# Kernel optimization log

Measured on AMD Instinct MI355X. Metric: run time of the kernel, lower is better.

The kernel has to match this reference:

```python
import jax, jax.numpy as jnp
import numpy as np

N, D, N_CLASSES = 8192, 512, 128
POS_MARGIN = 1.0  # default path: sample_method=None, Dynamic_margin=None


def setup_inputs() -> dict:
    key = jax.random.key(0)
    k1, k2 = jax.random.split(key)
    x = jax.random.normal(k1, (N, D), dtype=jnp.float32)
    # metric-learning embeddings are L2-normalized so sim in [-1, 1]
    x = x / jnp.linalg.norm(x, axis=1, keepdims=True)
    targets = jax.random.randint(k2, (N,), 0, N_CLASSES, dtype=jnp.int64)
    return {"inputs": x, "targets": targets, "nonorm": 0}


def reference(inputs, targets, nonorm):
    n = inputs.shape[0]
    sim = jnp.matmul(inputs, inputs.T)                      # [n, n]
    same = targets[:, None] == targets[None, :]             # [n, n]
    pos_mask = same & (sim < POS_MARGIN)                    # drops self-sim == 1
    neg_mask = ~same

    # per-row masked log-sum-exp (sort in original is irrelevant to the sums)
    pos_sum = jnp.sum(jnp.where(pos_mask, jnp.exp(1.0 - sim), 0.0), axis=1)
    neg_sum = jnp.sum(jnp.where(neg_mask, jnp.exp(sim), 0.0), axis=1)
    pos_loss = jnp.log(pos_sum)
    neg_loss = jnp.log(neg_sum)

    has_neg = jnp.any(neg_mask, axis=1)                     # rows w/o negs are skipped
    loss = jnp.sum(jnp.where(has_neg, pos_loss + neg_loss, 0.0)) / n
    prec = jnp.mean(1.0 - has_neg.astype(jnp.float32))      # fraction of skipped rows

    # torch code reports means of the LAST row's pos/neg pairs
    last_pos = pos_mask[-1]
    last_neg = neg_mask[-1]
    mean_pos_sim = jnp.sum(jnp.where(last_pos, sim[-1], 0.0)) / jnp.sum(last_pos)
    mean_neg_sim = jnp.sum(jnp.where(last_neg, sim[-1], 0.0)) / jnp.sum(last_neg)
    return loss, prec, mean_pos_sim, mean_neg_sim
```

## Files before the change

kernel.cpp:

```cpp
#include <hip/hip_runtime.h>
#include <math.h>

#define N_ 8192
#define D_ 512
#define NC_ 128
#define T_ 64
#define BK_ 32
#define KSTEPS 16

typedef __attribute__((ext_vector_type(8))) short bf16x8;
typedef __attribute__((ext_vector_type(4))) float f32x4;
typedef __attribute__((ext_vector_type(4))) unsigned short us4;

static __device__ __forceinline__ unsigned short f2bf(float f) {
    union { float f; unsigned u; } c; c.f = f;
    unsigned u = c.u;
    u += 0x7fffu + ((u >> 16) & 1u);
    return (unsigned short)(u >> 16);
}

__global__ __launch_bounds__(256) void k_pre(const float* __restrict__ x,
                                             unsigned short* __restrict__ xb,
                                             const int* __restrict__ tg,
                                             double* __restrict__ sim_last,
                                             int* __restrict__ hist32) {
    const int bid = blockIdx.x;
    const int tid = threadIdx.x;
    if (bid < 4096) {
        int i = bid * 256 + tid;
        float4 v = reinterpret_cast<const float4*>(x)[i];
        us4 o = { f2bf(v.x), f2bf(v.y), f2bf(v.z), f2bf(v.w) };
        reinterpret_cast<us4*>(xb)[i] = o;
    } else if (bid < 6144) {
        int j    = (bid - 4096) * 4 + (tid >> 6);
        int lane = tid & 63;
        const float* xl = x + (size_t)(N_ - 1) * D_;
        const float* xj = x + (size_t)j * D_;
        double acc = 0.0;
#pragma unroll
        for (int it = 0; it < 8; ++it) {
            int k = it * 64 + lane;
            acc += (double)xl[k] * (double)xj[k];
        }
#pragma unroll
        for (int m = 32; m >= 1; m >>= 1) acc += __shfl_xor(acc, m, 64);
        if (lane == 0) sim_last[j] = acc;
    } else {
        __shared__ int lh[NC_];
        int b = bid - 6144;
        if (tid < NC_) lh[tid] = 0;
        __syncthreads();
        atomicAdd(&lh[tg[b * 256 + tid]], 1);
        __syncthreads();
        if (tid < NC_) hist32[b * NC_ + tid] = lh[tid];
    }
}

__global__ __launch_bounds__(256, 4) void k_main(const unsigned short* __restrict__ xb,
                                                 const int* __restrict__ tg,
                                                 float* __restrict__ bufP,
                                                 float* __restrict__ bufN) {
    __shared__ alignas(16) unsigned short As[2][128 * BK_];
    __shared__ alignas(16) unsigned short Bs[2][128 * BK_];
    __shared__ int rowT[128];

    const int tid  = threadIdx.x;
    const int w    = tid >> 6;
    const int lane = tid & 63;
    const int q    = lane >> 4;
    const int l15  = lane & 15;
    const int wrow = w >> 1;
    const int wcol = w & 1;

    const int bswz = (blockIdx.x & 7) * 260 + (blockIdx.x >> 3);

    int rem = bswz;
    int it = 0;
    while (rem >= (T_ - it)) { rem -= (T_ - it); it++; }
    const int jt = it + rem;
    const int row0 = it * 128;
    const int col0 = jt * 128;

    auto STAGE = [&](int buf, int ks) {
        const int k0 = ks * BK_;
        unsigned short* Ad = As[buf];
        unsigned short* Bd = Bs[buf];
#pragma unroll
        for (int itr = 0; itr < 2; ++itr) {
            int slot = itr * 4 + w;
            int gs = slot * 64 + lane;
            int r  = gs >> 2;
            int sl = gs & 3;
            int g  = sl ^ ((r >> 1) & 3);
            const unsigned short* ga = xb + (size_t)(row0 + r) * D_ + k0 + g * 8;
            const unsigned short* gb = xb + (size_t)(col0 + r) * D_ + k0 + g * 8;
            __builtin_amdgcn_global_load_lds(
                (const __attribute__((address_space(1))) void*)ga,
                (__attribute__((address_space(3))) void*)(Ad + slot * 512),
                16, 0, 0);
            __builtin_amdgcn_global_load_lds(
                (const __attribute__((address_space(1))) void*)gb,
                (__attribute__((address_space(3))) void*)(Bd + slot * 512),
                16, 0, 0);
        }
    };

    if (tid < 128) rowT[tid] = tg[row0 + tid];
    STAGE(0, 0);
    __syncthreads();

    int tR[4][4];
#pragma unroll
    for (int mi = 0; mi < 4; ++mi)
#pragma unroll
        for (int r = 0; r < 4; ++r)
            tR[mi][r] = rowT[wrow * 64 + mi * 16 + q * 4 + r];

    int tC[4];
#pragma unroll
    for (int ni = 0; ni < 4; ++ni)
        tC[ni] = tg[col0 + wcol * 64 + ni * 16 + l15];

    f32x4 acc[4][4];
#pragma unroll
    for (int mi = 0; mi < 4; ++mi)
#pragma unroll
        for (int ni = 0; ni < 4; ++ni)
            acc[mi][ni] = (f32x4){0.f, 0.f, 0.f, 0.f};

    auto COMPUTE = [&](int buf) {
        const unsigned short* A = As[buf];
        const unsigned short* B = Bs[buf];
        bf16x8 aF[4], bF[4];
#pragma unroll
        for (int mi = 0; mi < 4; ++mi) {
            int rA = wrow * 64 + mi * 16 + l15;
            int sl = q ^ ((rA >> 1) & 3);
            aF[mi] = *reinterpret_cast<const bf16x8*>(A + rA * BK_ + sl * 8);
        }
#pragma unroll
        for (int ni = 0; ni < 4; ++ni) {
            int rB = wcol * 64 + ni * 16 + l15;
            int sl = q ^ ((rB >> 1) & 3);
            bF[ni] = *reinterpret_cast<const bf16x8*>(B + rB * BK_ + sl * 8);
        }
#pragma unroll
        for (int mi = 0; mi < 4; ++mi)
#pragma unroll
            for (int ni = 0; ni < 4; ++ni)
                acc[mi][ni] = __builtin_amdgcn_mfma_f32_16x16x32_bf16(
                    aF[mi], bF[ni], acc[mi][ni], 0, 0, 0);
    };

    int cur = 0;
#pragma unroll 1
    for (int ks = 0; ks < KSTEPS - 1; ++ks) {
        STAGE(cur ^ 1, ks + 1);
        COMPUTE(cur);
        __syncthreads();
        cur ^= 1;
    }
    COMPUTE(cur);

    float ps[4][4], ns[4][4];
    float cps[4], cns[4];
#pragma unroll
    for (int mi = 0; mi < 4; ++mi)
#pragma unroll
        for (int r = 0; r < 4; ++r) { ps[mi][r] = 0.f; ns[mi][r] = 0.f; }
#pragma unroll
    for (int ni = 0; ni < 4; ++ni) { cps[ni] = 0.f; cns[ni] = 0.f; }

#pragma unroll
    for (int mi = 0; mi < 4; ++mi)
#pragma unroll
        for (int ni = 0; ni < 4; ++ni)
#pragma unroll
            for (int r = 0; r < 4; ++r) {
                float s = acc[mi][ni][r];
                bool same = (tR[mi][r] == tC[ni]);
                float e = __expf(same ? 1.0f - s : s);
                float pe = (same && (s < 1.0f)) ? e : 0.0f;
                float ne = same ? 0.0f : e;
                ps[mi][r] += pe; ns[mi][r] += ne;
                cps[ni]   += pe; cns[ni]   += ne;
            }

    __syncthreads();
    float* scr = (float*)As;

#pragma unroll
    for (int mi = 0; mi < 4; ++mi)
#pragma unroll
        for (int r = 0; r < 4; ++r) {
            float p = ps[mi][r];
            float n = ns[mi][r];
#pragma unroll
            for (int m = 1; m < 16; m <<= 1) {
                p += __shfl_xor(p, m, 64);
                n += __shfl_xor(n, m, 64);
            }
            if (l15 == 0) {
                int rloc = wrow * 64 + mi * 16 + q * 4 + r;
                scr[wcol * 128 + rloc]       = p;
                scr[256 + wcol * 128 + rloc] = n;
            }
        }

#pragma unroll
    for (int ni = 0; ni < 4; ++ni) {
        float p = cps[ni];
        float n = cns[ni];
        p += __shfl_xor(p, 16, 64); p += __shfl_xor(p, 32, 64);
        n += __shfl_xor(n, 16, 64); n += __shfl_xor(n, 32, 64);
        if (q == 0) {
            int cloc = wcol * 64 + ni * 16 + l15;
            scr[512 + wrow * 128 + cloc] = p;
            scr[768 + wrow * 128 + cloc] = n;
        }
    }
    __syncthreads();

    if (tid < 128) {
        int r = tid;
        size_t off = ((size_t)it * T_ + jt) * 128 + r;
        bufP[off] = scr[r]       + scr[128 + r];
        bufN[off] = scr[256 + r] + scr[384 + r];
    } else if (jt != it) {
        int c = tid - 128;
        size_t off = ((size_t)jt * T_ + it) * 128 + c;
        bufP[off] = scr[512 + c] + scr[640 + c];
        bufN[off] = scr[768 + c] + scr[896 + c];
    }
}

__global__ __launch_bounds__(256) void k_reduce(const float* __restrict__ bufP,
                                                const float* __restrict__ bufN,
                                                const int* __restrict__ tg,
                                                const int* __restrict__ hist32,
                                                double* __restrict__ partd,
                                                int* __restrict__ skipc) {
    __shared__ float sv[256];
    __shared__ int lh[NC_];
    __shared__ double rd[128];
    __shared__ int ri[128];
    const int t   = blockIdx.x;
    const int tid = threadIdx.x;
    const int half = tid >> 7;
    const int r    = tid & 127;
    const float* buf = half ? bufN : bufP;
    const float* base = buf + (size_t)t * T_ * 128 + r;
    float s = 0.f;
#pragma unroll
    for (int o = 0; o < T_; ++o) s += base[o * 128];
    sv[tid] = s;
    if (tid < NC_) {
        int a = 0;
#pragma unroll
        for (int b = 0; b < 32; ++b) a += hist32[b * NC_ + tid];
        lh[tid] = a;
    }
    __syncthreads();
    if (tid < 128) {
        int row = t * 128 + tid;
        bool ok = lh[tg[row]] < N_;
        rd[tid] = ok ? (double)(logf(sv[tid]) + logf(sv[128 + tid])) : 0.0;
        ri[tid] = ok ? 0 : 1;
    }
    __syncthreads();
    for (int st = 64; st >= 1; st >>= 1) {
        if (tid < st) { rd[tid] += rd[tid + st]; ri[tid] += ri[tid + st]; }
        __syncthreads();
    }
    if (tid == 0) { partd[t] = rd[0]; skipc[t] = ri[0]; }
}

__global__ __launch_bounds__(1024) void k_final(const double* __restrict__ partd,
                                                const int* __restrict__ skipc,
                                                const int* __restrict__ tg,
                                                const double* __restrict__ sim_last,
                                                float* __restrict__ out) {
    __shared__ double sl[1024], sp[1024], sn[1024];
    __shared__ int    sk[1024], cp[1024], cn[1024];
    int tid = threadIdx.x;

    double part = (tid < 64) ? partd[tid] : 0.0;
    int    skip = (tid < 64) ? skipc[tid] : 0;

    double pd = 0.0, nd = 0.0;
    int pc = 0, nc = 0;
    int tlast = tg[N_ - 1];
    for (int j = tid; j < N_; j += 1024) {
        double s = sim_last[j];
        if (tg[j] == tlast) {
            if (s < 1.0) { pd += s; pc++; }
        } else {
            nd += s; nc++;
        }
    }

    sl[tid] = part; sk[tid] = skip;
    sp[tid] = pd;   cp[tid] = pc;
    sn[tid] = nd;   cn[tid] = nc;
    __syncthreads();
    for (int s = 512; s >= 1; s >>= 1) {
        if (tid < s) {
            sl[tid] += sl[tid + s]; sk[tid] += sk[tid + s];
            sp[tid] += sp[tid + s]; cp[tid] += cp[tid + s];
            sn[tid] += sn[tid + s]; cn[tid] += cn[tid + s];
        }
        __syncthreads();
    }
    if (tid == 0) {
        out[0] = (float)(sl[0] / (double)N_);
        out[1] = (float)sk[0] / (float)N_;
        out[2] = (float)(sp[0] / (double)cp[0]);
        out[3] = (float)(sn[0] / (double)cn[0]);
    }
}

extern "C" void kernel_launch(void* const* d_in, const int* in_sizes, int n_in,
                              void* d_out, int out_size, void* d_ws, size_t ws_size,
                              hipStream_t stream) {
    const float* x  = (const float*)d_in[0];
    const int*   tg = (const int*)d_in[1];
    char* ws = (char*)d_ws;

    unsigned short* xb = (unsigned short*)ws;
    const size_t XB = (size_t)N_ * D_ * 2;
    double* partd    = (double*)(ws + XB);
    int*    skipc    = (int*)(ws + XB + 512);
    int*    hist32   = (int*)(ws + XB + 1024);
    double* sim_last = (double*)(ws + XB + 65536);
    float*  bufP     = (float*)(ws + XB + 131072);
    float*  bufN     = (float*)(ws + XB + 131072 + 2097152);

    const int nblk_tri = T_ * (T_ + 1) / 2;

    hipLaunchKernelGGL(k_pre, dim3(4096 + 2048 + 32), dim3(256), 0, stream,
                       x, xb, tg, sim_last, hist32);
    hipLaunchKernelGGL(k_main, dim3(nblk_tri), dim3(256), 0, stream, xb, tg, bufP, bufN);
    hipLaunchKernelGGL(k_reduce, dim3(T_), dim3(256), 0, stream,
                       bufP, bufN, tg, hist32, partd, skipc);
    hipLaunchKernelGGL(k_final, dim3(1), dim3(1024), 0, stream,
                       partd, skipc, tg, sim_last, (float*)d_out);
}
```

Baseline: 152.8 us.

## Enlarge GEMM tiles to 256x256 with 512 threads and restructure post-reduction

The symmetric-triangle GEMM moves from 128x128 tiles with BK=32 to 256x256 tiles with BK=64, using 512 threads, 8x4 MFMA fragments per wave and a fully unrolled double-buffered pipeline. It adds explicit waitcnt, sched_barrier and setprio hints. The aim is to raise arithmetic intensity and cut global and LDS traffic per FLOP. The row/column reduction and last-row statistics are merged into one k_post kernel, and the final reduction uses wave shuffles. The risks are higher register pressure from 128 accumulator floats per lane, and fewer blocks (528) that may underfill the CUs.

```diff
diff --git a/kernel.cpp b/kernel.cpp
--- a/kernel.cpp
+++ b/kernel.cpp
@@ -4,9 +4,9 @@
 #define N_ 8192
 #define D_ 512
 #define NC_ 128
-#define T_ 64
-#define BK_ 32
-#define KSTEPS 16
+#define T32 32
+#define BK_ 64
+#define KSTEPS 8
 
 typedef __attribute__((ext_vector_type(8))) short bf16x8;
 typedef __attribute__((ext_vector_type(4))) float f32x4;
@@ -56,156 +56,155 @@
     }
 }
 
-__global__ __launch_bounds__(256, 4) void k_main(const unsigned short* __restrict__ xb,
+__global__ __launch_bounds__(512, 2) void k_main(const unsigned short* __restrict__ xb,
                                                  const int* __restrict__ tg,
                                                  float* __restrict__ bufP,
                                                  float* __restrict__ bufN) {
-    __shared__ alignas(16) unsigned short As[2][128 * BK_];
-    __shared__ alignas(16) unsigned short Bs[2][128 * BK_];
-    __shared__ int rowT[128];
+    __shared__ alignas(16) unsigned short As0_[2 * 256 * 64];
+    __shared__ alignas(16) unsigned short Bs0_[2 * 256 * 64];
 
     const int tid  = threadIdx.x;
     const int w    = tid >> 6;
     const int lane = tid & 63;
     const int q    = lane >> 4;
     const int l15  = lane & 15;
-    const int wrow = w >> 1;
-    const int wcol = w & 1;
-
-    const int bswz = (blockIdx.x & 7) * 260 + (blockIdx.x >> 3);
+    const int wrow = w >> 2;
+    const int wcol = w & 3;
+
+    const int bswz = (blockIdx.x & 7) * 66 + (blockIdx.x >> 3);
 
     int rem = bswz;
     int it = 0;
-    while (rem >= (T_ - it)) { rem -= (T_ - it); it++; }
+    while (rem >= (T32 - it)) { rem -= (T32 - it); it++; }
     const int jt = it + rem;
-    const int row0 = it * 128;
-    const int col0 = jt * 128;
-
-    auto STAGE = [&](int buf, int ks) {
-        const int k0 = ks * BK_;
-        unsigned short* Ad = As[buf];
-        unsigned short* Bd = Bs[buf];
-#pragma unroll
-        for (int itr = 0; itr < 2; ++itr) {
-            int slot = itr * 4 + w;
-            int gs = slot * 64 + lane;
-            int r  = gs >> 2;
-            int sl = gs & 3;
-            int g  = sl ^ ((r >> 1) & 3);
+    const int row0 = it * 256;
+    const int col0 = jt * 256;
+
+    auto stage_tile = [&](int p, int kt) {
+        const int k0 = kt * BK_;
+#pragma unroll
+        for (int set = 0; set < 4; ++set) {
+            int ls = set * 4096 + tid * 8;
+            int r  = ls >> 6;
+            int sl = (ls >> 3) & 7;
+            int g  = sl ^ (r & 7);
             const unsigned short* ga = xb + (size_t)(row0 + r) * D_ + k0 + g * 8;
             const unsigned short* gb = xb + (size_t)(col0 + r) * D_ + k0 + g * 8;
             __builtin_amdgcn_global_load_lds(
                 (const __attribute__((address_space(1))) void*)ga,
-                (__attribute__((address_space(3))) void*)(Ad + slot * 512),
+                (__attribute__((address_space(3))) void*)(As0_ + p * 16384 + set * 4096 + w * 512),
                 16, 0, 0);
             __builtin_amdgcn_global_load_lds(
                 (const __attribute__((address_space(1))) void*)gb,
-                (__attribute__((address_space(3))) void*)(Bd + slot * 512),
+                (__attribute__((address_space(3))) void*)(Bs0_ + p * 16384 + set * 4096 + w * 512),
                 16, 0, 0);
         }
     };
 
-    if (tid < 128) rowT[tid] = tg[row0 + tid];
-    STAGE(0, 0);
-    __syncthreads();
-
-    int tR[4][4];
-#pragma unroll
-    for (int mi = 0; mi < 4; ++mi)
-#pragma unroll
-        for (int r = 0; r < 4; ++r)
-            tR[mi][r] = rowT[wrow * 64 + mi * 16 + q * 4 + r];
-
-    int tC[4];
-#pragma unroll
-    for (int ni = 0; ni < 4; ++ni)
-        tC[ni] = tg[col0 + wcol * 64 + ni * 16 + l15];
-
-    f32x4 acc[4][4];
-#pragma unroll
-    for (int mi = 0; mi < 4; ++mi)
+    f32x4 acc[8][4];
+#pragma unroll
+    for (int mi = 0; mi < 8; ++mi)
 #pragma unroll
         for (int ni = 0; ni < 4; ++ni)
             acc[mi][ni] = (f32x4){0.f, 0.f, 0.f, 0.f};
 
-    auto COMPUTE = [&](int buf) {
-        const unsigned short* A = As[buf];
-        const unsigned short* B = Bs[buf];
-        bf16x8 aF[4], bF[4];
-#pragma unroll
-        for (int mi = 0; mi < 4; ++mi) {
-            int rA = wrow * 64 + mi * 16 + l15;
-            int sl = q ^ ((rA >> 1) & 3);
-            aF[mi] = *reinterpret_cast<const bf16x8*>(A + rA * BK_ + sl * 8);
+    auto compute_kc = [&](int p, int kc) {
+        bf16x8 aF[8], bF[4];
+#pragma unroll
+        for (int mi = 0; mi < 8; ++mi) {
+            int rA = wrow * 128 + mi * 16 + l15;
+            int sl = (kc * 4 + q) ^ (rA & 7);
+            aF[mi] = *reinterpret_cast<const bf16x8*>(As0_ + p * 16384 + rA * 64 + sl * 8);
         }
 #pragma unroll
         for (int ni = 0; ni < 4; ++ni) {
             int rB = wcol * 64 + ni * 16 + l15;
-            int sl = q ^ ((rB >> 1) & 3);
-            bF[ni] = *reinterpret_cast<const bf16x8*>(B + rB * BK_ + sl * 8);
-        }
-#pragma unroll
-        for (int mi = 0; mi < 4; ++mi)
+            int sl = (kc * 4 + q) ^ (rB & 7);
+            bF[ni] = *reinterpret_cast<const bf16x8*>(Bs0_ + p * 16384 + rB * 64 + sl * 8);
+        }
+        asm volatile("s_waitcnt lgkmcnt(0)" ::: "memory");
+        __builtin_amdgcn_sched_barrier(0);
+        __builtin_amdgcn_s_setprio(1);
+#pragma unroll
+        for (int mi = 0; mi < 8; ++mi)
 #pragma unroll
             for (int ni = 0; ni < 4; ++ni)
                 acc[mi][ni] = __builtin_amdgcn_mfma_f32_16x16x32_bf16(
                     aF[mi], bF[ni], acc[mi][ni], 0, 0, 0);
+        __builtin_amdgcn_s_setprio(0);
     };
 
-    int cur = 0;
-#pragma unroll 1
-    for (int ks = 0; ks < KSTEPS - 1; ++ks) {
-        STAGE(cur ^ 1, ks + 1);
-        COMPUTE(cur);
-        __syncthreads();
-        cur ^= 1;
-    }
-    COMPUTE(cur);
-
-    float ps[4][4], ns[4][4];
+#define TILE(P, KS, DOSTAGE, VMN)                                         \
+    do {                                                                  \
+        asm volatile("s_waitcnt vmcnt(" #VMN ")" ::: "memory");           \
+        __builtin_amdgcn_s_barrier();                                     \
+        __builtin_amdgcn_sched_barrier(0);                                \
+        compute_kc(P, 0);                                                 \
+        compute_kc(P, 1);                                                 \
+        __builtin_amdgcn_s_barrier();                                     \
+        if (DOSTAGE) stage_tile(P, (KS) + 2);                             \
+    } while (0)
+
+    stage_tile(0, 0);
+    stage_tile(1, 1);
+
+    TILE(0, 0, 1, 8);
+    TILE(1, 1, 1, 8);
+    TILE(0, 2, 1, 8);
+    TILE(1, 3, 1, 8);
+    TILE(0, 4, 1, 8);
+    TILE(1, 5, 1, 8);
+    TILE(0, 6, 0, 8);
+    TILE(1, 7, 0, 0);
+#undef TILE
+
+    int tC[4];
+#pragma unroll
+    for (int ni = 0; ni < 4; ++ni)
+        tC[ni] = tg[col0 + wcol * 64 + ni * 16 + l15];
+
     float cps[4], cns[4];
 #pragma unroll
-    for (int mi = 0; mi < 4; ++mi)
-#pragma unroll
-        for (int r = 0; r < 4; ++r) { ps[mi][r] = 0.f; ns[mi][r] = 0.f; }
-#pragma unroll
     for (int ni = 0; ni < 4; ++ni) { cps[ni] = 0.f; cns[ni] = 0.f; }
 
-#pragma unroll
-    for (int mi = 0; mi < 4; ++mi)
+    float* scr = (float*)As0_;
+
+#pragma unroll
+    for (int mi = 0; mi < 8; ++mi) {
+        int tRv[4];
+#pragma unroll
+        for (int r = 0; r < 4; ++r)
+            tRv[r] = tg[row0 + wrow * 128 + mi * 16 + q * 4 + r];
+        float ps_[4] = {0.f, 0.f, 0.f, 0.f};
+        float ns_[4] = {0.f, 0.f, 0.f, 0.f};
 #pragma unroll
         for (int ni = 0; ni < 4; ++ni)
 #pragma unroll
             for (int r = 0; r < 4; ++r) {
                 float s = acc[mi][ni][r];
-                bool same = (tR[mi][r] == tC[ni]);
+                bool same = (tRv[r] == tC[ni]);
                 float e = __expf(same ? 1.0f - s : s);
                 float pe = (same && (s < 1.0f)) ? e : 0.0f;
                 float ne = same ? 0.0f : e;
-                ps[mi][r] += pe; ns[mi][r] += ne;
-                cps[ni]   += pe; cns[ni]   += ne;
+                ps_[r] += pe; ns_[r] += ne;
+                cps[ni] += pe; cns[ni] += ne;
             }
-
-    __syncthreads();
-    float* scr = (float*)As;
-
-#pragma unroll
-    for (int mi = 0; mi < 4; ++mi)
 #pragma unroll
         for (int r = 0; r < 4; ++r) {
-            float p = ps[mi][r];
-            float n = ns[mi][r];
+            float p = ps_[r];
+            float n = ns_[r];
 #pragma unroll
             for (int m = 1; m < 16; m <<= 1) {
                 p += __shfl_xor(p, m, 64);
                 n += __shfl_xor(n, m, 64);
             }
             if (l15 == 0) {
-                int rloc = wrow * 64 + mi * 16 + q * 4 + r;
-                scr[wcol * 128 + rloc]       = p;
-                scr[256 + wcol * 128 + rloc] = n;
+                int rloc = wrow * 128 + mi * 16 + q * 4 + r;
+                scr[wcol * 256 + rloc]        = p;
+                scr[1024 + wcol * 256 + rloc] = n;
             }
         }
+    }
 
 #pragma unroll
     for (int ni = 0; ni < 4; ++ni) {
@@ -215,44 +214,45 @@
         n += __shfl_xor(n, 16, 64); n += __shfl_xor(n, 32, 64);
         if (q == 0) {
             int cloc = wcol * 64 + ni * 16 + l15;
-            scr[512 + wrow * 128 + cloc] = p;
-            scr[768 + wrow * 128 + cloc] = n;
+            scr[2048 + wrow * 256 + cloc] = p;
+            scr[2560 + wrow * 256 + cloc] = n;
         }
     }
     __syncthreads();
 
-    if (tid < 128) {
+    if (tid < 256) {
         int r = tid;
-        size_t off = ((size_t)it * T_ + jt) * 128 + r;
-        bufP[off] = scr[r]       + scr[128 + r];
-        bufN[off] = scr[256 + r] + scr[384 + r];
+        size_t off = ((size_t)it * T32 + jt) * 256 + r;
+        bufP[off] = scr[r] + scr[256 + r] + scr[512 + r] + scr[768 + r];
+        bufN[off] = scr[1024 + r] + scr[1280 + r] + scr[1536 + r] + scr[1792 + r];
     } else if (jt != it) {
-        int c = tid - 128;
-        size_t off = ((size_t)jt * T_ + it) * 128 + c;
-        bufP[off] = scr[512 + c] + scr[640 + c];
-        bufN[off] = scr[768 + c] + scr[896 + c];
-    }
-}
-
-__global__ __launch_bounds__(256) void k_reduce(const float* __restrict__ bufP,
-                                                const float* __restrict__ bufN,
-                                                const int* __restrict__ tg,
-                                                const int* __restrict__ hist32,
-                                                double* __restrict__ partd,
-                                                int* __restrict__ skipc) {
-    __shared__ float sv[256];
+        int c = tid - 256;
+        size_t off = ((size_t)jt * T32 + it) * 256 + c;
+        bufP[off] = scr[2048 + c] + scr[2304 + c];
+        bufN[off] = scr[2560 + c] + scr[2816 + c];
+    }
+}
+
+__global__ __launch_bounds__(512) void k_post(const float* __restrict__ bufP,
+                                              const float* __restrict__ bufN,
+                                              const int* __restrict__ tg,
+                                              const int* __restrict__ hist32,
+                                              const double* __restrict__ sim_last,
+                                              double* __restrict__ dpart,
+                                              int* __restrict__ ipart) {
+    __shared__ float sv[512];
     __shared__ int lh[NC_];
-    __shared__ double rd[128];
-    __shared__ int ri[128];
-    const int t   = blockIdx.x;
+    __shared__ double Rd[512], Pd[512], Nd[512];
+    __shared__ int Ri[512], Pc[512], Nc[512];
+    const int rt  = blockIdx.x;
     const int tid = threadIdx.x;
-    const int half = tid >> 7;
-    const int r    = tid & 127;
-    const float* buf = half ? bufN : bufP;
-    const float* base = buf + (size_t)t * T_ * 128 + r;
+    const int half = tid >> 8;
+    const int r    = tid & 255;
+    const float* buf  = half ? bufN : bufP;
+    const float* base = buf + (size_t)rt * T32 * 256 + r;
     float s = 0.f;
 #pragma unroll
-    for (int o = 0; o < T_; ++o) s += base[o * 128];
+    for (int o = 0; o < T32; ++o) s += base[o * 256];
     sv[tid] = s;
     if (tid < NC_) {
         int a = 0;
@@ -261,61 +261,56 @@
         lh[tid] = a;
     }
     __syncthreads();
-    if (tid < 128) {
-        int row = t * 128 + tid;
+    double rd = 0.0, pd = 0.0, nd = 0.0;
+    int ri = 0, pc = 0, nc = 0;
+    if (tid < 256) {
+        int row = rt * 256 + tid;
         bool ok = lh[tg[row]] < N_;
-        rd[tid] = ok ? (double)(logf(sv[tid]) + logf(sv[128 + tid])) : 0.0;
-        ri[tid] = ok ? 0 : 1;
-    }
+        rd = ok ? (double)(logf(sv[tid]) + logf(sv[256 + tid])) : 0.0;
+        ri = ok ? 0 : 1;
+        double sl = sim_last[row];
+        int tlast = tg[N_ - 1];
+        if (tg[row] == tlast) { if (sl < 1.0) { pd = sl; pc = 1; } }
+        else                  { nd = sl; nc = 1; }
+    }
+    Rd[tid] = rd; Pd[tid] = pd; Nd[tid] = nd;
+    Ri[tid] = ri; Pc[tid] = pc; Nc[tid] = nc;
     __syncthreads();
-    for (int st = 64; st >= 1; st >>= 1) {
-        if (tid < st) { rd[tid] += rd[tid + st]; ri[tid] += ri[tid + st]; }
+    for (int st = 256; st >= 1; st >>= 1) {
+        if (tid < st) {
+            Rd[tid] += Rd[tid + st]; Pd[tid] += Pd[tid + st]; Nd[tid] += Nd[tid + st];
+            Ri[tid] += Ri[tid + st]; Pc[tid] += Pc[tid + st]; Nc[tid] += Nc[tid + st];
+        }
         __syncthreads();
     }
-    if (tid == 0) { partd[t] = rd[0]; skipc[t] = ri[0]; }
-}
-
-__global__ __launch_bounds__(1024) void k_final(const double* __restrict__ partd,
-                                                const int* __restrict__ skipc,
-                                                const int* __restrict__ tg,
-                                                const double* __restrict__ sim_last,
-                                                float* __restrict__ out) {
-    __shared__ double sl[1024], sp[1024], sn[1024];
-    __shared__ int    sk[1024], cp[1024], cn[1024];
+    if (tid == 0) {
+        dpart[rt] = Rd[0]; dpart[32 + rt] = Pd[0]; dpart[64 + rt] = Nd[0];
+        ipart[rt] = Ri[0]; ipart[32 + rt] = Pc[0]; ipart[64 + rt] = Nc[0];
+    }
+}
+
+__global__ __launch_bounds__(64) void k_fin(const double* __restrict__ dpart,
+                                            const int* __restrict__ ipart,
+                                            float* __restrict__ out) {
     int tid = threadIdx.x;
-
-    double part = (tid < 64) ? partd[tid] : 0.0;
-    int    skip = (tid < 64) ? skipc[tid] : 0;
-
-    double pd = 0.0, nd = 0.0;
-    int pc = 0, nc = 0;
-    int tlast = tg[N_ - 1];
-    for (int j = tid; j < N_; j += 1024) {
-        double s = sim_last[j];
-        if (tg[j] == tlast) {
-            if (s < 1.0) { pd += s; pc++; }
-        } else {
-            nd += s; nc++;
-        }
-    }
-
-    sl[tid] = part; sk[tid] = skip;
-    sp[tid] = pd;   cp[tid] = pc;
-    sn[tid] = nd;   cn[tid] = nc;
-    __syncthreads();
-    for (int s = 512; s >= 1; s >>= 1) {
-        if (tid < s) {
-            sl[tid] += sl[tid + s]; sk[tid] += sk[tid + s];
-            sp[tid] += sp[tid + s]; cp[tid] += cp[tid + s];
-            sn[tid] += sn[tid + s]; cn[tid] += cn[tid + s];
-        }
-        __syncthreads();
+    double rd = tid < 32 ? dpart[tid]      : 0.0;
+    double pd = tid < 32 ? dpart[32 + tid] : 0.0;
+    double nd = tid < 32 ? dpart[64 + tid] : 0.0;
+    int    ri = tid < 32 ? ipart[tid]      : 0;
+    int    pc = tid < 32 ? ipart[32 + tid] : 0;
+    int    nc = tid < 32 ? ipart[64 + tid] : 0;
+#pragma unroll
+    for (int m = 32; m >= 1; m >>= 1) {
+        rd += __shfl_xor(rd, m, 64); pd += __shfl_xor(pd, m, 64);
+        nd += __shfl_xor(nd, m, 64);
+        ri += __shfl_xor(ri, m, 64); pc += __shfl_xor(pc, m, 64);
+        nc += __shfl_xor(nc, m, 64);
     }
     if (tid == 0) {
-        out[0] = (float)(sl[0] / (double)N_);
-        out[1] = (float)sk[0] / (float)N_;
-        out[2] = (float)(sp[0] / (double)cp[0]);
-        out[3] = (float)(sn[0] / (double)cn[0]);
+        out[0] = (float)(rd / (double)N_);
+        out[1] = (float)ri / (float)N_;
+        out[2] = (float)(pd / (double)pc);
+        out[3] = (float)(nd / (double)nc);
     }
 }
 
@@ -328,20 +323,19 @@
 
     unsigned short* xb = (unsigned short*)ws;
     const size_t XB = (size_t)N_ * D_ * 2;
-    double* partd    = (double*)(ws + XB);
-    int*    skipc    = (int*)(ws + XB + 512);
-    int*    hist32   = (int*)(ws + XB + 1024);
-    double* sim_last = (double*)(ws + XB + 65536);
-    float*  bufP     = (float*)(ws + XB + 131072);
-    float*  bufN     = (float*)(ws + XB + 131072 + 2097152);
-
-    const int nblk_tri = T_ * (T_ + 1) / 2;
+    float*  bufP     = (float*)(ws + XB);
+    float*  bufN     = (float*)(ws + XB + (1u << 20));
+    double* sim_last = (double*)(ws + XB + (2u << 20));
+    int*    hist32   = (int*)(ws + XB + (2u << 20) + 65536);
+    double* dpart    = (double*)(ws + XB + (2u << 20) + 65536 + 16384);
+    int*    ipart    = (int*)(ws + XB + (2u << 20) + 65536 + 16384 + 1024);
+
+    const int nblk_tri = T32 * (T32 + 1) / 2;
 
     hipLaunchKernelGGL(k_pre, dim3(4096 + 2048 + 32), dim3(256), 0, stream,
                        x, xb, tg, sim_last, hist32);
-    hipLaunchKernelGGL(k_main, dim3(nblk_tri), dim3(256), 0, stream, xb, tg, bufP, bufN);
-    hipLaunchKernelGGL(k_reduce, dim3(T_), dim3(256), 0, stream,
-                       bufP, bufN, tg, hist32, partd, skipc);
-    hipLaunchKernelGGL(k_final, dim3(1), dim3(1024), 0, stream,
-                       partd, skipc, tg, sim_last, (float*)d_out);
-}
+    hipLaunchKernelGGL(k_main, dim3(nblk_tri), dim3(512), 0, stream, xb, tg, bufP, bufN);
+    hipLaunchKernelGGL(k_post, dim3(T32), dim3(512), 0, stream,
+                       bufP, bufN, tg, hist32, sim_last, dpart, ipart);
+    hipLaunchKernelGGL(k_fin, dim3(1), dim3(64), 0, stream, dpart, ipart, (float*)d_out);
+}
```

Measured after the change: 157.4 us. 3.0% more time.
